# Kernel tuning notes

Hardware: AMD Instinct MI355X
Metric: run time of the kernel (lower is better)

## Reference

```python
import jax, jax.numpy as jnp
import numpy as np

# Module hyperparams (from init_kwargs)
B, C, F, K, H, W = 8, 32, 32, 3, 32, 32
Q = K * K          # kernel positions
PAD = K // 2       # 'same' padding (output spatial == input spatial)
# groups = in_channels (num_groups=None default) -> step = 1, weight axis = F*Q*C


def setup_inputs() -> dict:
    key = jax.random.key(0)
    k1, k2, k3 = jax.random.split(key, 3)
    x = jax.random.normal(k1, (B, C, H, W), dtype=jnp.float32)
    # learned per-weight rational coefficients: one rational per (f, kernel_pos, channel)
    nums = jax.random.normal(k2, (F * Q * C, 6), dtype=jnp.float32) * 0.1
    denoms = jax.random.normal(k3, (F * Q * C, 4), dtype=jnp.float32) * 0.1
    return {"x": x, "nums": nums, "denoms": denoms}


def reference(x, nums, denoms):
    # per-weight Pade rational activation over conv windows, scatter-accumulated
    # into output channels:
    #   out[b,f,y,x] = sum_{q in KxK, c} P_{f,q,c}(w) / (1 + |D_{f,q,c}(w)|),
    #   w = zero-padded input at window position q, channel c.
    a = nums.reshape(F, Q, C, 6)    # numerator coeffs, powers 0..5
    b = denoms.reshape(F, Q, C, 4)  # denominator coeffs, powers 1..4

    xp = jnp.pad(x, ((0, 0), (0, 0), (PAD, PAD), (PAD, PAD)))
    # gather K*K shifted views: [B, C, Q, H, W]
    win = jnp.stack([xp[:, :, i:i + H, j:j + W]
                     for i in range(K) for j in range(K)], axis=2)

    # powers w^0..w^5: [B, C, Q, 6, H, W]
    w1 = win
    w2 = w1 * w1
    w3 = w2 * w1
    w4 = w2 * w2
    w5 = w4 * w1
    pows = jnp.stack([jnp.ones_like(w1), w1, w2, w3, w4, w5], axis=3)

    # numerator P and denominator D, per (f, q, c): [B, F, Q, C, H, W]
    num = jnp.einsum('bcqphw,fqcp->bfqchw', pows, a)
    den = 1.0 + jnp.abs(jnp.einsum('bcqphw,fqcp->bfqchw', pows[:, :, :, 1:5], b))

    # accumulate over kernel positions and channels -> [B, F, H, W]
    return jnp.sum(num / den, axis=(2, 3))
```

## Files before the change

### kernel.cpp

```cpp
#include <hip/hip_runtime.h>
#include <math.h>

#define NB 8
#define NC 32
#define NF 32
#define NH 32
#define NW 32
#define NQ 9
#define CSPLIT 4
#define CPB (NC / CSPLIT)
#define TROWS 18
#define TS 34
#define TILE_N (TROWS * TS)

typedef float f2 __attribute__((ext_vector_type(2)));
__device__ __forceinline__ f2 sp(float v) { return (f2){v, v}; }

__global__ __launch_bounds__(256, 8) void ka_conv_rational_kernel(
    const float* __restrict__ x,
    const float* __restrict__ nums,
    const float* __restrict__ dens,
    float* __restrict__ out)
{
    __shared__ float tile[2][TILE_N];

    const int t    = threadIdx.x;
    const int bid  = blockIdx.x;
    const int cs   = bid & (CSPLIT - 1);
    const int half = (bid >> 2) & 1;
    const int bf   = bid >> 3;
    const int f    = bf & (NF - 1);
    const int bb   = bf >> 5;
    const int xx   = t & 31;
    const int ty   = t >> 5;
    const int c0   = cs * CPB;

    int  soff[3];
    bool svalid[3];
#pragma unroll
    for (int i = 0; i < 3; ++i) {
        int idx = t + i * 256;
        int ry  = idx / TS;
        int rx  = idx - ry * TS;
        int gy  = half * 16 + ry - 1;
        int gx  = rx - 1;
        bool ok = (idx < TILE_N) && (gy >= 0) && (gy < NH) && (gx >= 0) && (gx < NW);
        svalid[i] = ok;
        soff[i]   = ok ? (gy * NW + gx) : 0;
    }

    const float* __restrict__ xb    = x    + ((size_t)bb * NC + c0) * NH * NW;
    const float* __restrict__ abase = nums + (size_t)f * NQ * NC * 6;
    const float* __restrict__ bbase = dens + (size_t)f * NQ * NC * 4;

    float st[3];
#pragma unroll
    for (int i = 0; i < 3; ++i)
        st[i] = xb[soff[i]];

    f2 acc = {0.f, 0.f};

    for (int ci = 0; ci < CPB; ++ci) {
        const int c = c0 + ci;
        float* tl = tile[ci & 1];

#pragma unroll
        for (int i = 0; i < 3; ++i) {
            int idx = t + i * 256;
            if (idx < TILE_N)
                tl[idx] = svalid[i] ? st[i] : 0.f;
        }
        if (ci + 1 < CPB) {
            const float* xc = xb + (size_t)(ci + 1) * NH * NW;
#pragma unroll
            for (int i = 0; i < 3; ++i)
                st[i] = xc[soff[i]];
        }
        __syncthreads();

        float n[4][3];
#pragma unroll
        for (int dy = 0; dy < 4; ++dy)
#pragma unroll
            for (int dx = 0; dx < 3; ++dx)
                n[dy][dx] = tl[(ty * 2 + dy) * TS + (xx + dx)];

#pragma unroll
        for (int q = 0; q < NQ; ++q) {
            const float* ap = abase + (size_t)(q * NC + c) * 6;
            const float* bp = bbase + (size_t)(q * NC + c) * 4;
            const float a0 = ap[0], a1 = ap[1], a2 = ap[2],
                        a3 = ap[3], a4 = ap[4], a5 = ap[5];
            const float d0 = bp[0], d1 = bp[1], d2 = bp[2], d3 = bp[3];
            const int qi = q / 3, qj = q - qi * 3;

            f2 w = {n[qi][qj], n[qi + 1][qj]};
            f2 nu = __builtin_elementwise_fma(sp(a5), w, sp(a4));
            nu = __builtin_elementwise_fma(nu, w, sp(a3));
            nu = __builtin_elementwise_fma(nu, w, sp(a2));
            nu = __builtin_elementwise_fma(nu, w, sp(a1));
            nu = __builtin_elementwise_fma(nu, w, sp(a0));
            f2 dp = __builtin_elementwise_fma(sp(d3), w, sp(d2));
            dp = __builtin_elementwise_fma(dp, w, sp(d1));
            dp = __builtin_elementwise_fma(dp, w, sp(d0));
            dp = dp * w;
            f2 de = 1.0f + __builtin_elementwise_abs(dp);
            f2 r  = {__builtin_amdgcn_rcpf(de.x), __builtin_amdgcn_rcpf(de.y)};
            acc = __builtin_elementwise_fma(nu, r, acc);
        }
    }

    const int y0 = half * 16 + ty * 2;
    float* op = out + ((size_t)bf * NH + y0) * NW + xx;
    unsafeAtomicAdd(op, acc.x);
    unsafeAtomicAdd(op + NW, acc.y);
}

extern "C" void kernel_launch(void* const* d_in, const int* in_sizes, int n_in,
                              void* d_out, int out_size, void* d_ws, size_t ws_size,
                              hipStream_t stream) {
    const float* x    = (const float*)d_in[0];
    const float* nums = (const float*)d_in[1];
    const float* dens = (const float*)d_in[2];
    float* out = (float*)d_out;

    hipMemsetAsync(d_out, 0, (size_t)out_size * sizeof(float), stream);

    dim3 grid(NB * NF * 2 * CSPLIT);
    dim3 block(256);
    ka_conv_rational_kernel<<<grid, block, 0, stream>>>(x, nums, dens, out);
}
```

Measured before the change: 82.13 us.

## Stage all channel tiles in LDS upfront and share one reciprocal per pair

```diff
diff --git a/kernel.cpp b/kernel.cpp
--- a/kernel.cpp
+++ b/kernel.cpp
@@ -22,7 +22,7 @@
     const float* __restrict__ dens,
     float* __restrict__ out)
 {
-    __shared__ float tile[2][TILE_N];
+    __shared__ float tile[CPB][TILE_N];
 
     const int t    = threadIdx.x;
     const int bid  = blockIdx.x;
@@ -49,34 +49,30 @@
         soff[i]   = ok ? (gy * NW + gx) : 0;
     }
 
-    const float* __restrict__ xb    = x    + ((size_t)bb * NC + c0) * NH * NW;
+    const float* __restrict__ xb = x + ((size_t)bb * NC + c0) * NH * NW;
+
+#pragma unroll
+    for (int g = 0; g < CPB; ++g) {
+        const float* __restrict__ xc = xb + g * (NH * NW);
+        float v0 = xc[soff[0]];
+        float v1 = xc[soff[1]];
+        float v2 = xc[soff[2]];
+        tile[g][t]       = svalid[0] ? v0 : 0.f;
+        tile[g][t + 256] = svalid[1] ? v1 : 0.f;
+        if (t + 512 < TILE_N)
+            tile[g][t + 512] = svalid[2] ? v2 : 0.f;
+    }
+    __syncthreads();
+
     const float* __restrict__ abase = nums + (size_t)f * NQ * NC * 6;
     const float* __restrict__ bbase = dens + (size_t)f * NQ * NC * 4;
 
-    float st[3];
-#pragma unroll
-    for (int i = 0; i < 3; ++i)
-        st[i] = xb[soff[i]];
-
     f2 acc = {0.f, 0.f};
 
+#pragma unroll 2
     for (int ci = 0; ci < CPB; ++ci) {
         const int c = c0 + ci;
-        float* tl = tile[ci & 1];
-
-#pragma unroll
-        for (int i = 0; i < 3; ++i) {
-            int idx = t + i * 256;
-            if (idx < TILE_N)
-                tl[idx] = svalid[i] ? st[i] : 0.f;
-        }
-        if (ci + 1 < CPB) {
-            const float* xc = xb + (size_t)(ci + 1) * NH * NW;
-#pragma unroll
-            for (int i = 0; i < 3; ++i)
-                st[i] = xc[soff[i]];
-        }
-        __syncthreads();
+        const float* __restrict__ tl = tile[ci];
 
         float n[4][3];
 #pragma unroll
@@ -105,7 +101,11 @@
             dp = __builtin_elementwise_fma(dp, w, sp(d0));
             dp = dp * w;
             f2 de = 1.0f + __builtin_elementwise_abs(dp);
-            f2 r  = {__builtin_amdgcn_rcpf(de.x), __builtin_amdgcn_rcpf(de.y)};
+            float pr = de.x * de.y;
+            float rr = __builtin_amdgcn_rcpf(pr);
+            f2 r;
+            r.x = de.y * rr;
+            r.y = de.x * rr;
             acc = __builtin_elementwise_fma(nu, r, acc);
         }
     }
```

Measured after the change: 87.61 us. 1.07x slower.

## Compute full image per block with four rows per thread, split channels eightfold

Applied to the files above, without the earlier changes.

```diff
diff --git a/kernel.cpp b/kernel.cpp
--- a/kernel.cpp
+++ b/kernel.cpp
@@ -7,9 +7,9 @@
 #define NH 32
 #define NW 32
 #define NQ 9
-#define CSPLIT 4
+#define CSPLIT 8
 #define CPB (NC / CSPLIT)
-#define TROWS 18
+#define TROWS 34
 #define TS 34
 #define TILE_N (TROWS * TS)
 
@@ -24,25 +24,24 @@
 {
     __shared__ float tile[2][TILE_N];
 
-    const int t    = threadIdx.x;
-    const int bid  = blockIdx.x;
-    const int cs   = bid & (CSPLIT - 1);
-    const int half = (bid >> 2) & 1;
-    const int bf   = bid >> 3;
-    const int f    = bf & (NF - 1);
-    const int bb   = bf >> 5;
-    const int xx   = t & 31;
-    const int ty   = t >> 5;
-    const int c0   = cs * CPB;
+    const int t   = threadIdx.x;
+    const int bid = blockIdx.x;
+    const int cs  = bid & (CSPLIT - 1);
+    const int bf  = bid >> 3;
+    const int f   = bf & (NF - 1);
+    const int bb  = bf >> 5;
+    const int xx  = t & 31;
+    const int ty  = t >> 5;
+    const int c0  = cs * CPB;
 
-    int  soff[3];
-    bool svalid[3];
+    int  soff[5];
+    bool svalid[5];
 #pragma unroll
-    for (int i = 0; i < 3; ++i) {
+    for (int i = 0; i < 5; ++i) {
         int idx = t + i * 256;
         int ry  = idx / TS;
         int rx  = idx - ry * TS;
-        int gy  = half * 16 + ry - 1;
+        int gy  = ry - 1;
         int gx  = rx - 1;
         bool ok = (idx < TILE_N) && (gy >= 0) && (gy < NH) && (gx >= 0) && (gx < NW);
         svalid[i] = ok;
@@ -53,19 +52,20 @@
     const float* __restrict__ abase = nums + (size_t)f * NQ * NC * 6;
     const float* __restrict__ bbase = dens + (size_t)f * NQ * NC * 4;
 
-    float st[3];
+    float st[5];
 #pragma unroll
-    for (int i = 0; i < 3; ++i)
+    for (int i = 0; i < 5; ++i)
         st[i] = xb[soff[i]];
 
-    f2 acc = {0.f, 0.f};
+    f2 acc01 = {0.f, 0.f};
+    f2 acc23 = {0.f, 0.f};
 
     for (int ci = 0; ci < CPB; ++ci) {
         const int c = c0 + ci;
         float* tl = tile[ci & 1];
 
 #pragma unroll
-        for (int i = 0; i < 3; ++i) {
+        for (int i = 0; i < 5; ++i) {
             int idx = t + i * 256;
             if (idx < TILE_N)
                 tl[idx] = svalid[i] ? st[i] : 0.f;
@@ -73,17 +73,17 @@
         if (ci + 1 < CPB) {
             const float* xc = xb + (size_t)(ci + 1) * NH * NW;
 #pragma unroll
-            for (int i = 0; i < 3; ++i)
+            for (int i = 0; i < 5; ++i)
                 st[i] = xc[soff[i]];
         }
         __syncthreads();
 
-        float n[4][3];
+        float n[6][3];
 #pragma unroll
-        for (int dy = 0; dy < 4; ++dy)
+        for (int dy = 0; dy < 6; ++dy)
 #pragma unroll
             for (int dx = 0; dx < 3; ++dx)
-                n[dy][dx] = tl[(ty * 2 + dy) * TS + (xx + dx)];
+                n[dy][dx] = tl[(ty * 4 + dy) * TS + (xx + dx)];
 
 #pragma unroll
         for (int q = 0; q < NQ; ++q) {
@@ -94,26 +94,44 @@
             const float d0 = bp[0], d1 = bp[1], d2 = bp[2], d3 = bp[3];
             const int qi = q / 3, qj = q - qi * 3;
 
-            f2 w = {n[qi][qj], n[qi + 1][qj]};
-            f2 nu = __builtin_elementwise_fma(sp(a5), w, sp(a4));
-            nu = __builtin_elementwise_fma(nu, w, sp(a3));
-            nu = __builtin_elementwise_fma(nu, w, sp(a2));
-            nu = __builtin_elementwise_fma(nu, w, sp(a1));
-            nu = __builtin_elementwise_fma(nu, w, sp(a0));
-            f2 dp = __builtin_elementwise_fma(sp(d3), w, sp(d2));
-            dp = __builtin_elementwise_fma(dp, w, sp(d1));
-            dp = __builtin_elementwise_fma(dp, w, sp(d0));
-            dp = dp * w;
-            f2 de = 1.0f + __builtin_elementwise_abs(dp);
-            f2 r  = {__builtin_amdgcn_rcpf(de.x), __builtin_amdgcn_rcpf(de.y)};
-            acc = __builtin_elementwise_fma(nu, r, acc);
+            f2 w01 = {n[qi][qj],     n[qi + 1][qj]};
+            f2 w23 = {n[qi + 2][qj], n[qi + 3][qj]};
+
+            f2 nu01 = __builtin_elementwise_fma(sp(a5), w01, sp(a4));
+            f2 nu23 = __builtin_elementwise_fma(sp(a5), w23, sp(a4));
+            nu01 = __builtin_elementwise_fma(nu01, w01, sp(a3));
+            nu23 = __builtin_elementwise_fma(nu23, w23, sp(a3));
+            nu01 = __builtin_elementwise_fma(nu01, w01, sp(a2));
+            nu23 = __builtin_elementwise_fma(nu23, w23, sp(a2));
+            nu01 = __builtin_elementwise_fma(nu01, w01, sp(a1));
+            nu23 = __builtin_elementwise_fma(nu23, w23, sp(a1));
+            nu01 = __builtin_elementwise_fma(nu01, w01, sp(a0));
+            nu23 = __builtin_elementwise_fma(nu23, w23, sp(a0));
+
+            f2 dp01 = __builtin_elementwise_fma(sp(d3), w01, sp(d2));
+            f2 dp23 = __builtin_elementwise_fma(sp(d3), w23, sp(d2));
+            dp01 = __builtin_elementwise_fma(dp01, w01, sp(d1));
+            dp23 = __builtin_elementwise_fma(dp23, w23, sp(d1));
+            dp01 = __builtin_elementwise_fma(dp01, w01, sp(d0));
+            dp23 = __builtin_elementwise_fma(dp23, w23, sp(d0));
+            dp01 = dp01 * w01;
+            dp23 = dp23 * w23;
+
+            f2 de01 = 1.0f + __builtin_elementwise_abs(dp01);
+            f2 de23 = 1.0f + __builtin_elementwise_abs(dp23);
+            f2 r01 = {__builtin_amdgcn_rcpf(de01.x), __builtin_amdgcn_rcpf(de01.y)};
+            f2 r23 = {__builtin_amdgcn_rcpf(de23.x), __builtin_amdgcn_rcpf(de23.y)};
+            acc01 = __builtin_elementwise_fma(nu01, r01, acc01);
+            acc23 = __builtin_elementwise_fma(nu23, r23, acc23);
         }
     }
 
-    const int y0 = half * 16 + ty * 2;
+    const int y0 = ty * 4;
     float* op = out + ((size_t)bf * NH + y0) * NW + xx;
-    unsafeAtomicAdd(op, acc.x);
-    unsafeAtomicAdd(op + NW, acc.y);
+    unsafeAtomicAdd(op,          acc01.x);
+    unsafeAtomicAdd(op + NW,     acc01.y);
+    unsafeAtomicAdd(op + 2 * NW, acc23.x);
+    unsafeAtomicAdd(op + 3 * NW, acc23.y);
 }
 
 extern "C" void kernel_launch(void* const* d_in, const int* in_sizes, int n_in,
@@ -126,7 +144,7 @@
 
     hipMemsetAsync(d_out, 0, (size_t)out_size * sizeof(float), stream);
 
-    dim3 grid(NB * NF * 2 * CSPLIT);
+    dim3 grid(NB * NF * CSPLIT);
     dim3 block(256);
     ka_conv_rational_kernel<<<grid, block, 0, stream>>>(x, nums, dens, out);
 }
```

After: 79.77 us. 1.03x faster.

## Map lanes to input channels and reduce with shuffles instead of atomics

Applied to the files above, without the earlier changes.

```diff
diff --git a/kernel.cpp b/kernel.cpp
--- a/kernel.cpp
+++ b/kernel.cpp
@@ -7,14 +7,8 @@
 #define NH 32
 #define NW 32
 #define NQ 9
-#define CSPLIT 4
-#define CPB (NC / CSPLIT)
-#define TROWS 18
-#define TS 34
-#define TILE_N (TROWS * TS)
-
-typedef float f2 __attribute__((ext_vector_type(2)));
-__device__ __forceinline__ f2 sp(float v) { return (f2){v, v}; }
+#define FSPLIT 8
+#define FPB 4
 
 __global__ __launch_bounds__(256, 8) void ka_conv_rational_kernel(
     const float* __restrict__ x,
@@ -22,98 +16,104 @@
     const float* __restrict__ dens,
     float* __restrict__ out)
 {
-    __shared__ float tile[2][TILE_N];
+    __shared__ float xt[NC][3][NW + 2];
 
-    const int t    = threadIdx.x;
-    const int bid  = blockIdx.x;
-    const int cs   = bid & (CSPLIT - 1);
-    const int half = (bid >> 2) & 1;
-    const int bf   = bid >> 3;
-    const int f    = bf & (NF - 1);
-    const int bb   = bf >> 5;
-    const int xx   = t & 31;
-    const int ty   = t >> 5;
-    const int c0   = cs * CPB;
-
-    int  soff[3];
-    bool svalid[3];
-#pragma unroll
-    for (int i = 0; i < 3; ++i) {
-        int idx = t + i * 256;
-        int ry  = idx / TS;
-        int rx  = idx - ry * TS;
-        int gy  = half * 16 + ry - 1;
-        int gx  = rx - 1;
-        bool ok = (idx < TILE_N) && (gy >= 0) && (gy < NH) && (gx >= 0) && (gx < NW);
-        svalid[i] = ok;
-        soff[i]   = ok ? (gy * NW + gx) : 0;
-    }
-
-    const float* __restrict__ xb    = x    + ((size_t)bb * NC + c0) * NH * NW;
-    const float* __restrict__ abase = nums + (size_t)f * NQ * NC * 6;
-    const float* __restrict__ bbase = dens + (size_t)f * NQ * NC * 4;
-
-    float st[3];
-#pragma unroll
-    for (int i = 0; i < 3; ++i)
-        st[i] = xb[soff[i]];
-
-    f2 acc = {0.f, 0.f};
-
-    for (int ci = 0; ci < CPB; ++ci) {
-        const int c = c0 + ci;
-        float* tl = tile[ci & 1];
+    const int t   = threadIdx.x;
+    const int bid = blockIdx.x;
+    const int fq  = bid & (FSPLIT - 1);
+    const int y   = (bid >> 3) & (NH - 1);
+    const int b   = bid >> 8;
 
 #pragma unroll
-        for (int i = 0; i < 3; ++i) {
-            int idx = t + i * 256;
-            if (idx < TILE_N)
-                tl[idx] = svalid[i] ? st[i] : 0.f;
+    for (int i = 0; i < 12; ++i) {
+        int e   = t + i * 256;
+        int c   = e >> 5;
+        int ri  = c - (c / 3) * 3;
+        (void)ri;
+        int cc  = e / 96;
+        int rem = e - cc * 96;
+        int rr  = rem >> 5;
+        int col = rem & 31;
+        int gy  = y - 1 + rr;
+        float v = (gy >= 0 && gy < NH)
+                      ? x[(((size_t)b * NC + cc) * NH + gy) * NW + col]
+                      : 0.f;
+        xt[cc][rr][col + 1] = v;
+    }
+    if (t < 96) {
+        int cc = t / 3, rr = t - (t / 3) * 3;
+        xt[cc][rr][0] = 0.f;
+    } else if (t >= 128 && t < 224) {
+        int u = t - 128;
+        int cc = u / 3, rr = u - (u / 3) * 3;
+        xt[cc][rr][33] = 0.f;
+    }
+    __syncthreads();
+
+    const int lane = t & 63;
+    const int c    = lane & 31;
+    const int sl   = lane >> 5;
+    const int wv   = t >> 6;
+    const int f    = fq * FPB + wv;
+
+    const float* __restrict__ nbase = nums + ((size_t)f * NQ * NC + c) * 6;
+    const float* __restrict__ dbase = dens + ((size_t)f * NQ * NC + c) * 4;
+
+    float acc[16];
+#pragma unroll
+    for (int i = 0; i < 16; ++i) acc[i] = 0.f;
+
+    float A0 = nbase[0], A1 = nbase[1], A2 = nbase[2],
+          A3 = nbase[3], A4 = nbase[4], A5 = nbase[5];
+    float D0 = dbase[0], D1 = dbase[1], D2 = dbase[2], D3 = dbase[3];
+
+#pragma unroll 1
+    for (int q = 0; q < NQ; ++q) {
+        const float a0 = A0, a1 = A1, a2 = A2, a3 = A3, a4 = A4, a5 = A5;
+        const float d0 = D0, d1 = D1, d2 = D2, d3 = D3;
+        if (q + 1 < NQ) {
+            const float* nn = nbase + (size_t)(q + 1) * NC * 6;
+            const float* dn = dbase + (size_t)(q + 1) * NC * 4;
+            A0 = nn[0]; A1 = nn[1]; A2 = nn[2];
+            A3 = nn[3]; A4 = nn[4]; A5 = nn[5];
+            D0 = dn[0]; D1 = dn[1]; D2 = dn[2]; D3 = dn[3];
         }
-        if (ci + 1 < CPB) {
-            const float* xc = xb + (size_t)(ci + 1) * NH * NW;
-#pragma unroll
-            for (int i = 0; i < 3; ++i)
-                st[i] = xc[soff[i]];
-        }
-        __syncthreads();
-
-        float n[4][3];
-#pragma unroll
-        for (int dy = 0; dy < 4; ++dy)
-#pragma unroll
-            for (int dx = 0; dx < 3; ++dx)
-                n[dy][dx] = tl[(ty * 2 + dy) * TS + (xx + dx)];
+        const int qi = q / 3, qj = q - qi * 3;
+        const float* wrow = &xt[c][qi][qj + sl];
 
 #pragma unroll
-        for (int q = 0; q < NQ; ++q) {
-            const float* ap = abase + (size_t)(q * NC + c) * 6;
-            const float* bp = bbase + (size_t)(q * NC + c) * 4;
-            const float a0 = ap[0], a1 = ap[1], a2 = ap[2],
-                        a3 = ap[3], a4 = ap[4], a5 = ap[5];
-            const float d0 = bp[0], d1 = bp[1], d2 = bp[2], d3 = bp[3];
-            const int qi = q / 3, qj = q - qi * 3;
-
-            f2 w = {n[qi][qj], n[qi + 1][qj]};
-            f2 nu = __builtin_elementwise_fma(sp(a5), w, sp(a4));
-            nu = __builtin_elementwise_fma(nu, w, sp(a3));
-            nu = __builtin_elementwise_fma(nu, w, sp(a2));
-            nu = __builtin_elementwise_fma(nu, w, sp(a1));
-            nu = __builtin_elementwise_fma(nu, w, sp(a0));
-            f2 dp = __builtin_elementwise_fma(sp(d3), w, sp(d2));
-            dp = __builtin_elementwise_fma(dp, w, sp(d1));
-            dp = __builtin_elementwise_fma(dp, w, sp(d0));
-            dp = dp * w;
-            f2 de = 1.0f + __builtin_elementwise_abs(dp);
-            f2 r  = {__builtin_amdgcn_rcpf(de.x), __builtin_amdgcn_rcpf(de.y)};
-            acc = __builtin_elementwise_fma(nu, r, acc);
+        for (int it = 0; it < 16; ++it) {
+            float w  = wrow[it * 2];
+            float nu = fmaf(a5, w, a4);
+            nu = fmaf(nu, w, a3);
+            nu = fmaf(nu, w, a2);
+            nu = fmaf(nu, w, a1);
+            nu = fmaf(nu, w, a0);
+            float dd = fmaf(d3, w, d2);
+            dd = fmaf(dd, w, d1);
+            dd = fmaf(dd, w, d0);
+            dd *= w;
+            float de = 1.0f + fabsf(dd);
+            acc[it] = fmaf(nu, __builtin_amdgcn_rcpf(de), acc[it]);
         }
     }
 
-    const int y0 = half * 16 + ty * 2;
-    float* op = out + ((size_t)bf * NH + y0) * NW + xx;
-    unsafeAtomicAdd(op, acc.x);
-    unsafeAtomicAdd(op + NW, acc.y);
+#pragma unroll
+    for (int it = 0; it < 16; ++it) {
+        float v = acc[it];
+        v += __shfl_xor(v, 1, 64);
+        v += __shfl_xor(v, 2, 64);
+        v += __shfl_xor(v, 4, 64);
+        v += __shfl_xor(v, 8, 64);
+        v += __shfl_xor(v, 16, 64);
+        acc[it] = v;
+    }
+
+    float* op = out + (((size_t)b * NF + f) * NH + y) * NW;
+#pragma unroll
+    for (int it = 0; it < 16; ++it)
+        if (c == it)
+            op[it * 2 + sl] = acc[it];
 }
 
 extern "C" void kernel_launch(void* const* d_in, const int* in_sizes, int n_in,
@@ -124,9 +124,7 @@
     const float* dens = (const float*)d_in[2];
     float* out = (float*)d_out;
 
-    hipMemsetAsync(d_out, 0, (size_t)out_size * sizeof(float), stream);
-
-    dim3 grid(NB * NF * 2 * CSPLIT);
+    dim3 grid(NB * NH * FSPLIT);
     dim3 block(256);
     ka_conv_rational_kernel<<<grid, block, 0, stream>>>(x, nums, dens, out);
 }
```

After: 85.66 us. +4.3%, slower.
